# Kernel optimization log

Hardware: AMD Instinct MI355X
Metric: run time of the kernel (lower is better)

## Reference

```python
import math
import jax, jax.numpy as jnp
import numpy as np

HEAD_DIM = 128
SKETCH_DIM = 256  # multiple of 8, no padding needed in pack
_BIT_WEIGHTS = jnp.array([1, 2, 4, 8, 16, 32, 64, 128], dtype=jnp.uint8)


def _pack_bits(bits):
    # bits: uint8 0/1, trailing dim = SKETCH_DIM (multiple of 8)
    *lead, d = bits.shape
    b = bits.reshape(*lead, d // 8, 8)
    return (b * _BIT_WEIGHTS).sum(axis=-1).astype(jnp.uint8)


def _unpack_bits(packed, out_dim):
    # packed: uint8 [..., n] -> float32 [..., out_dim] of 0/1
    shifts = jnp.arange(8, dtype=jnp.uint8)
    bits = (packed[..., None] >> shifts) & jnp.uint8(1)
    bits = bits.reshape(*packed.shape[:-1], -1)[..., :out_dim]
    return bits.astype(jnp.float32)


def setup_inputs() -> dict:
    key = jax.random.key(0)
    kq, kk, kg = jax.random.split(key, 3)
    q = jax.random.normal(kq, (4, 32, 16, HEAD_DIM), dtype=jnp.float32)
    k = jax.random.normal(kk, (4, 32, 8192, HEAD_DIM), dtype=jnp.float32)
    G = jax.random.normal(kg, (HEAD_DIM, SKETCH_DIM), dtype=jnp.float32) / math.sqrt(SKETCH_DIM)
    return {"q": q, "k": k, "G": G}


def reference(q, k, G):
    # project_query: q @ G -> [B, H, Q, sketch_dim]
    q_sketch = jnp.einsum('bhqd,ds->bhqs', q, G)
    # sketch_key: sign-quantize k @ G, pack into uint8
    proj = jnp.einsum('bhkd,ds->bhks', k, G)
    bits = (proj > 0).astype(jnp.uint8)
    k_packed = _pack_bits(bits)  # [B, H, K, sketch_dim//8] uint8
    # estimate_scores: unpack to +/-1, dequant matmul, unbiasing scale
    k_signs = _unpack_bits(k_packed, SKETCH_DIM) * 2.0 - 1.0
    est = jnp.einsum('bhqs,bhks->bhqk', q_sketch, k_signs.astype(q_sketch.dtype))
    return est * jnp.float32(math.sqrt(math.pi / 2))
```

## Files before the change

kernel.cpp:

```cpp
#include <hip/hip_runtime.h>
#include <math.h>

typedef _Float16 f16;
typedef _Float16 f16x4 __attribute__((ext_vector_type(4)));
typedef _Float16 f16x8 __attribute__((ext_vector_type(8)));
typedef float    f32x4 __attribute__((ext_vector_type(4)));
typedef unsigned int u32;
typedef unsigned long long u64;

#define NHEADS 128
#define KLEN   8192
#define DDIM   128
#define SDIM   256
#define NROWS  (NHEADS * KLEN)
#define SCALE  1.2533141373155003f
#define TAU    2e-5f

#define QS_OFF     0
#define GFH_OFF    (1u << 20)
#define GFL_OFF    ((1u << 20) + (64u << 10))
#define GT_OFF     ((1u << 20) + (128u << 10))
#define PACKED_OFF (2u << 20)

__device__ __forceinline__ float seq_dot_np(const float* __restrict__ a,
                                            const float* __restrict__ gcol) {
  float acc = 0.0f;
  #pragma unroll 8
  for (int d = 0; d < DDIM; ++d)
    acc = __builtin_fmaf(a[d], gcol[d], acc);
  return acc;
}

__global__ void prep_qs_kernel(const float* __restrict__ q,
                               const float* __restrict__ G,
                               f16* __restrict__ qs16) {
  int idx = blockIdx.x * 256 + threadIdx.x;
  int s  = idx & 255;
  int hq = idx >> 8;
  const float* qr = q + (size_t)hq * DDIM;
  float acc = 0.f;
  #pragma unroll 8
  for (int d = 0; d < DDIM; ++d) acc += qr[d] * G[d * SDIM + s];
  qs16[idx] = (f16)acc;
}

__global__ void prep_g_kernel(const float* __restrict__ G,
                              f16* __restrict__ gfh, f16* __restrict__ gfl,
                              float* __restrict__ gt) {
  int t = blockIdx.x * 256 + threadIdx.x;
  int tl   = t >> 8;
  int c    = (t >> 6) & 3;
  int lane = t & 63;
  int s  = tl * 16 + (lane & 15);
  int d0 = c * 32 + (lane >> 4) * 8;
  f16x8 hh, ll;
  #pragma unroll
  for (int j = 0; j < 8; ++j) {
    float g = G[(size_t)(d0 + j) * SDIM + s];
    f16 h = (f16)g;
    hh[j] = h;
    ll[j] = (f16)((g - (float)h) * 4096.0f);
    gt[(size_t)s * DDIM + d0 + j] = g;
  }
  *(f16x8*)(gfh + (size_t)t * 8) = hh;
  *(f16x8*)(gfl + (size_t)t * 8) = ll;
}

__launch_bounds__(512, 1)
__global__ void proj_sign_kernel(const float* __restrict__ kmat,
                                 const f16* __restrict__ gfh,
                                 const f16* __restrict__ gfl,
                                 u32* __restrict__ packed,
                                 u32* __restrict__ smask) {
  __shared__ __align__(16) f16 lds[2][2][4][64][8];

  const int tid  = threadIdx.x;
  const int lane = tid & 63;
  const int w    = tid >> 6;
  const int g4 = lane >> 4;
  const int ln = lane & 15;
  const size_t rowbase = (size_t)blockIdx.x * 256;

  f16x8 Gh[2][4], Gl[2][4];
  #pragma unroll
  for (int mt = 0; mt < 2; ++mt)
    #pragma unroll
    for (int kc = 0; kc < 4; ++kc) {
      size_t o = ((size_t)((w * 2 + mt) * 4 + kc) * 64 + lane) * 8;
      Gh[mt][kc] = *(const f16x8*)(gfh + o);
      Gl[mt][kc] = *(const f16x8*)(gfl + o);
    }

  const int srl = tid >> 5;
  const int sd0 = (tid & 31) * 4;
  const int skc = sd0 >> 5;
  const int slf = srl | (((sd0 >> 3) & 3) << 4);
  const int sj0 = sd0 & 7;
  const float* kp = kmat + (rowbase + srl) * DDIM + sd0;

  {
    float4 rv = *(const float4*)kp;
    f16 h;
    f16x4 h4, l4;
    h = (f16)rv.x; h4[0] = h; l4[0] = (f16)((rv.x - (float)h) * 4096.0f);
    h = (f16)rv.y; h4[1] = h; l4[1] = (f16)((rv.y - (float)h) * 4096.0f);
    h = (f16)rv.z; h4[2] = h; l4[2] = (f16)((rv.z - (float)h) * 4096.0f);
    h = (f16)rv.w; h4[3] = h; l4[3] = (f16)((rv.w - (float)h) * 4096.0f);
    *(f16x4*)&lds[0][0][skc][slf][sj0] = h4;
    *(f16x4*)&lds[0][1][skc][slf][sj0] = l4;
  }
  __syncthreads();

  for (int t = 0; t < 16; ++t) {
    const int cb = t & 1;
    float4 rn;
    if (t < 15)
      rn = *(const float4*)(kp + (size_t)(t + 1) * 16 * DDIM);

    f32x4 ah0 = {0,0,0,0}, aa0 = {0,0,0,0}, ab0 = {0,0,0,0};
    f32x4 ah1 = {0,0,0,0}, aa1 = {0,0,0,0}, ab1 = {0,0,0,0};
    #pragma unroll
    for (int kc = 0; kc < 4; ++kc) {
      f16x8 Bh = *(const f16x8*)&lds[cb][0][kc][lane][0];
      f16x8 Bl = *(const f16x8*)&lds[cb][1][kc][lane][0];
      ah0 = __builtin_amdgcn_mfma_f32_16x16x32_f16(Gh[0][kc], Bh, ah0, 0, 0, 0);
      aa0 = __builtin_amdgcn_mfma_f32_16x16x32_f16(Gh[0][kc], Bl, aa0, 0, 0, 0);
      ab0 = __builtin_amdgcn_mfma_f32_16x16x32_f16(Gl[0][kc], Bh, ab0, 0, 0, 0);
      ah1 = __builtin_amdgcn_mfma_f32_16x16x32_f16(Gh[1][kc], Bh, ah1, 0, 0, 0);
      aa1 = __builtin_amdgcn_mfma_f32_16x16x32_f16(Gh[1][kc], Bl, aa1, 0, 0, 0);
      ab1 = __builtin_amdgcn_mfma_f32_16x16x32_f16(Gl[1][kc], Bh, ab1, 0, 0, 0);
    }
    float p[2][4];
    #pragma unroll
    for (int r = 0; r < 4; ++r) {
      p[0][r] = ah0[r] + (aa0[r] + ab0[r]) * 2.44140625e-4f;
      p[1][r] = ah1[r] + (aa1[r] + ab1[r]) * 2.44140625e-4f;
    }

    u32 pbits = 0, sbits = 0;
    #pragma unroll
    for (int mt = 0; mt < 2; ++mt)
      #pragma unroll
      for (int r = 0; r < 4; ++r)
        if (p[mt][r] > 0.0f) pbits |= (1u << (mt * 16 + g4 * 4 + r));
    float mn = __builtin_fabsf(p[0][0]);
    #pragma unroll
    for (int mt = 0; mt < 2; ++mt)
      #pragma unroll
      for (int r = 0; r < 4; ++r)
        mn = fminf(mn, __builtin_fabsf(p[mt][r]));
    if (__any(mn < TAU ? 1 : 0)) {
      #pragma unroll
      for (int mt = 0; mt < 2; ++mt)
        #pragma unroll
        for (int r = 0; r < 4; ++r)
          if (__builtin_fabsf(p[mt][r]) < TAU) sbits |= (1u << (mt * 16 + g4 * 4 + r));
    }
    pbits |= __shfl_xor(pbits, 16);  pbits |= __shfl_xor(pbits, 32);
    sbits |= __shfl_xor(sbits, 16);  sbits |= __shfl_xor(sbits, 32);
    if (lane < 16) {
      size_t row = rowbase + (size_t)t * 16 + ln;
      packed[row * 8 + w] = pbits;
      smask [row * 8 + w] = sbits;
    }

    if (t < 15) {
      f16 h;
      f16x4 h4, l4;
      h = (f16)rn.x; h4[0] = h; l4[0] = (f16)((rn.x - (float)h) * 4096.0f);
      h = (f16)rn.y; h4[1] = h; l4[1] = (f16)((rn.y - (float)h) * 4096.0f);
      h = (f16)rn.z; h4[2] = h; l4[2] = (f16)((rn.z - (float)h) * 4096.0f);
      h = (f16)rn.w; h4[3] = h; l4[3] = (f16)((rn.w - (float)h) * 4096.0f);
      *(f16x4*)&lds[1 - cb][0][skc][slf][sj0] = h4;
      *(f16x4*)&lds[1 - cb][1][skc][slf][sj0] = l4;
      __syncthreads();
    }
  }
}

__global__ void fixup_kernel(const float* __restrict__ kmat,
                             const float* __restrict__ gt,
                             u32* __restrict__ packed,
                             const u32* __restrict__ smask) {
  int row = blockIdx.x * 256 + threadIdx.x;
  if (row >= NROWS) return;
  const u32* mp = smask + (size_t)row * 8;
  uint4 m0 = *(const uint4*)mp;
  uint4 m1 = *(const uint4*)(mp + 4);
  u32 mw[8] = {m0.x, m0.y, m0.z, m0.w, m1.x, m1.y, m1.z, m1.w};
  if (!(mw[0] | mw[1] | mw[2] | mw[3] | mw[4] | mw[5] | mw[6] | mw[7])) return;
  const float* a = kmat + (size_t)row * DDIM;
  #pragma unroll
  for (int wd = 0; wd < 8; ++wd) {
    u32 m = mw[wd];
    if (!m) continue;
    u32 pk = packed[(size_t)row * 8 + wd];
    while (m) {
      int b = __ffs(m) - 1;  m &= m - 1;
      int s = wd * 32 + b;
      float acc = seq_dot_np(a, gt + (size_t)s * DDIM);
      if (acc > 0.0f) pk |= (1u << b);
      else            pk &= ~(1u << b);
    }
    packed[(size_t)row * 8 + wd] = pk;
  }
}

__launch_bounds__(256)
__global__ void est_kernel(const f16* __restrict__ qs16,
                           const u32* __restrict__ packed,
                           float* __restrict__ out) {
  const int tid  = threadIdx.x;
  const int lane = tid & 63;
  const int w    = tid >> 6;
  const int wg   = blockIdx.x;
  const int head   = wg >> 5;
  const int kchunk = (wg & 31) * 256;
  const int g4 = lane >> 4, ln = lane & 15;

  f16x8 aq[8];
  const f16* qb = qs16 + (size_t)head * 16 * SDIM;
  #pragma unroll
  for (int c = 0; c < 8; ++c)
    aq[c] = *(const f16x8*)(qb + ln * SDIM + c * 32 + g4 * 8);

  const int kb = kchunk + w * 64;
  #pragma unroll
  for (int kt = 0; kt < 4; ++kt) {
    int krow = kb + kt * 16 + ln;
    const u32* bp = packed + (size_t)(head * KLEN + krow) * 8;
    uint4 q0 = *(const uint4*)bp;
    uint4 q1 = *(const uint4*)(bp + 4);
    u32 b32[8] = {q0.x, q0.y, q0.z, q0.w, q1.x, q1.y, q1.z, q1.w};
    f32x4 acc = {0, 0, 0, 0};
    #pragma unroll
    for (int c = 0; c < 8; ++c) {
      u32 byte8 = (b32[c] >> (8 * g4)) & 0xffu;
      union { u32 u[4]; f16x8 h; } sv;
      #pragma unroll
      for (int pp = 0; pp < 4; ++pp) {
        u32 v = 0x3C003C00u;
        v |= ((byte8 >> (2 * pp))     & 1u) ? 0u : 0x8000u;
        v |= ((byte8 >> (2 * pp + 1)) & 1u) ? 0u : 0x80000000u;
        sv.u[pp] = v;
      }
      acc = __builtin_amdgcn_mfma_f32_16x16x32_f16(aq[c], sv.h, acc, 0, 0, 0);
    }
    float* ob = out + (size_t)(head * 16) * KLEN + kb + kt * 16 + ln;
    #pragma unroll
    for (int r = 0; r < 4; ++r) {
      int qrow = g4 * 4 + r;
      ob[(size_t)qrow * KLEN] = acc[r] * SCALE;
    }
  }
}

extern "C" void kernel_launch(void* const* d_in, const int* in_sizes, int n_in,
                              void* d_out, int out_size, void* d_ws, size_t ws_size,
                              hipStream_t stream) {
  const float* q = (const float*)d_in[0];
  const float* k = (const float*)d_in[1];
  const float* G = (const float*)d_in[2];
  float* out = (float*)d_out;
  char* ws = (char*)d_ws;

  f16*   qs16   = (f16*)(ws + QS_OFF);
  f16*   gfh    = (f16*)(ws + GFH_OFF);
  f16*   gfl    = (f16*)(ws + GFL_OFF);
  float* gt     = (float*)(ws + GT_OFF);
  u32*   packed = (u32*)(ws + PACKED_OFF);

  u32* smask = (u32*)d_out;

  prep_qs_kernel<<<2048, 256, 0, stream>>>(q, G, qs16);
  prep_g_kernel<<<16, 256, 0, stream>>>(G, gfh, gfl, gt);
  proj_sign_kernel<<<4096, 512, 0, stream>>>(k, gfh, gfl, packed, smask);
  fixup_kernel<<<4096, 256, 0, stream>>>(k, gt, packed, smask);
  est_kernel<<<4096, 256, 0, stream>>>(qs16, packed, out);
}
```

Measured before the change: 319.0 us.

## Split proj_sign blocks across sketch halves with 256-thread blocks

Each proj_sign block now handles only half of the sketch columns (4 waves instead of 8), with twice as many blocks covering both halves. Each thread stages 8 k values per row step instead of 4. The aim is finer-grained scheduling and higher occupancy under launch_bounds with 1 block. The cost is that every k tile is now read and converted to f16 hi/lo twice, once per half, which doubles k traffic and conversion work.

```diff
diff --git a/kernel.cpp b/kernel.cpp
--- a/kernel.cpp
+++ b/kernel.cpp
@@ -66,7 +66,7 @@
   *(f16x8*)(gfl + (size_t)t * 8) = ll;
 }
 
-__launch_bounds__(512, 1)
+__launch_bounds__(256, 1)
 __global__ void proj_sign_kernel(const float* __restrict__ kmat,
                                  const f16* __restrict__ gfh,
                                  const f16* __restrict__ gfl,
@@ -79,43 +79,51 @@
   const int w    = tid >> 6;
   const int g4 = lane >> 4;
   const int ln = lane & 15;
-  const size_t rowbase = (size_t)blockIdx.x * 256;
+  const int shalf = blockIdx.x & 1;
+  const size_t rowbase = (size_t)(blockIdx.x >> 1) * 256;
+  const int wout = shalf * 4 + w;
 
   f16x8 Gh[2][4], Gl[2][4];
   #pragma unroll
   for (int mt = 0; mt < 2; ++mt)
     #pragma unroll
     for (int kc = 0; kc < 4; ++kc) {
-      size_t o = ((size_t)((w * 2 + mt) * 4 + kc) * 64 + lane) * 8;
+      int tls = shalf * 8 + w * 2 + mt;
+      size_t o = ((size_t)(tls * 4 + kc) * 64 + lane) * 8;
       Gh[mt][kc] = *(const f16x8*)(gfh + o);
       Gl[mt][kc] = *(const f16x8*)(gfl + o);
     }
 
-  const int srl = tid >> 5;
-  const int sd0 = (tid & 31) * 4;
+  const int srl = tid >> 4;
+  const int sd0 = (tid & 15) * 8;
   const int skc = sd0 >> 5;
   const int slf = srl | (((sd0 >> 3) & 3) << 4);
-  const int sj0 = sd0 & 7;
   const float* kp = kmat + (rowbase + srl) * DDIM + sd0;
 
   {
-    float4 rv = *(const float4*)kp;
-    f16 h;
-    f16x4 h4, l4;
-    h = (f16)rv.x; h4[0] = h; l4[0] = (f16)((rv.x - (float)h) * 4096.0f);
-    h = (f16)rv.y; h4[1] = h; l4[1] = (f16)((rv.y - (float)h) * 4096.0f);
-    h = (f16)rv.z; h4[2] = h; l4[2] = (f16)((rv.z - (float)h) * 4096.0f);
-    h = (f16)rv.w; h4[3] = h; l4[3] = (f16)((rv.w - (float)h) * 4096.0f);
-    *(f16x4*)&lds[0][0][skc][slf][sj0] = h4;
-    *(f16x4*)&lds[0][1][skc][slf][sj0] = l4;
+    float4 a0 = *(const float4*)kp;
+    float4 a1 = *(const float4*)(kp + 4);
+    float af[8] = {a0.x, a0.y, a0.z, a0.w, a1.x, a1.y, a1.z, a1.w};
+    f16x8 h8, l8;
+    #pragma unroll
+    for (int j = 0; j < 8; ++j) {
+      f16 h = (f16)af[j];
+      h8[j] = h;
+      l8[j] = (f16)((af[j] - (float)h) * 4096.0f);
+    }
+    *(f16x8*)&lds[0][0][skc][slf][0] = h8;
+    *(f16x8*)&lds[0][1][skc][slf][0] = l8;
   }
   __syncthreads();
 
   for (int t = 0; t < 16; ++t) {
     const int cb = t & 1;
-    float4 rn;
-    if (t < 15)
-      rn = *(const float4*)(kp + (size_t)(t + 1) * 16 * DDIM);
+    float4 a0, a1;
+    if (t < 15) {
+      const float* np_ = kp + (size_t)(t + 1) * 16 * DDIM;
+      a0 = *(const float4*)np_;
+      a1 = *(const float4*)(np_ + 4);
+    }
 
     f32x4 ah0 = {0,0,0,0}, aa0 = {0,0,0,0}, ab0 = {0,0,0,0};
     f32x4 ah1 = {0,0,0,0}, aa1 = {0,0,0,0}, ab1 = {0,0,0,0};
@@ -160,19 +168,21 @@
     sbits |= __shfl_xor(sbits, 16);  sbits |= __shfl_xor(sbits, 32);
     if (lane < 16) {
       size_t row = rowbase + (size_t)t * 16 + ln;
-      packed[row * 8 + w] = pbits;
-      smask [row * 8 + w] = sbits;
+      packed[row * 8 + wout] = pbits;
+      smask [row * 8 + wout] = sbits;
     }
 
     if (t < 15) {
-      f16 h;
-      f16x4 h4, l4;
-      h = (f16)rn.x; h4[0] = h; l4[0] = (f16)((rn.x - (float)h) * 4096.0f);
-      h = (f16)rn.y; h4[1] = h; l4[1] = (f16)((rn.y - (float)h) * 4096.0f);
-      h = (f16)rn.z; h4[2] = h; l4[2] = (f16)((rn.z - (float)h) * 4096.0f);
-      h = (f16)rn.w; h4[3] = h; l4[3] = (f16)((rn.w - (float)h) * 4096.0f);
-      *(f16x4*)&lds[1 - cb][0][skc][slf][sj0] = h4;
-      *(f16x4*)&lds[1 - cb][1][skc][slf][sj0] = l4;
+      float af[8] = {a0.x, a0.y, a0.z, a0.w, a1.x, a1.y, a1.z, a1.w};
+      f16x8 h8, l8;
+      #pragma unroll
+      for (int j = 0; j < 8; ++j) {
+        f16 h = (f16)af[j];
+        h8[j] = h;
+        l8[j] = (f16)((af[j] - (float)h) * 4096.0f);
+      }
+      *(f16x8*)&lds[1 - cb][0][skc][slf][0] = h8;
+      *(f16x8*)&lds[1 - cb][1][skc][slf][0] = l8;
       __syncthreads();
     }
   }
@@ -274,7 +284,7 @@
 
   prep_qs_kernel<<<2048, 256, 0, stream>>>(q, G, qs16);
   prep_g_kernel<<<16, 256, 0, stream>>>(G, gfh, gfl, gt);
-  proj_sign_kernel<<<4096, 512, 0, stream>>>(k, gfh, gfl, packed, smask);
+  proj_sign_kernel<<<8192, 256, 0, stream>>>(k, gfh, gfl, packed, smask);
   fixup_kernel<<<4096, 256, 0, stream>>>(k, gt, packed, smask);
   est_kernel<<<4096, 256, 0, stream>>>(qs16, packed, out);
 }
```

Result: slower. 394.5 us (+23.7%).
